# Kernel optimization log

Hardware: AMD Instinct MI355X
Metric: run time of the kernel (lower is better)

The kernel has to match this reference:

```python
import jax, jax.numpy as jnp
import numpy as np

B, D, H = 65536, 1024, 8
HD = D // H


def setup_inputs() -> dict:
    key = jax.random.key(0)
    ks = jax.random.split(key, 6)
    s = 0.02  # init scale for weights
    return {
        "feat_a": jax.random.normal(ks[0], (B, D), jnp.float32),
        "feat_b": jax.random.normal(ks[1], (B, D), jnp.float32),
        "w_in_ab": jax.random.normal(ks[2], (3 * D, D), jnp.float32) * s,
        "b_in_ab": jnp.zeros((3 * D,), jnp.float32),
        "w_out_ab": jax.random.normal(ks[3], (D, D), jnp.float32) * s,
        "b_out_ab": jnp.zeros((D,), jnp.float32),
        "w_in_ba": jax.random.normal(ks[4], (3 * D, D), jnp.float32) * s,
        "b_in_ba": jnp.zeros((3 * D,), jnp.float32),
        "w_out_ba": jax.random.normal(ks[5], (D, D), jnp.float32) * s,
        "b_out_ba": jnp.zeros((D,), jnp.float32),
    }


def _mha_len1(q_in, kv_in, w_in, b_in, w_out, b_out):
    """PyTorch nn.MultiheadAttention math specialized to seq_len == 1 (eval mode).
    q_in, kv_in: [B, D]. Returns [B, D]."""
    wq, wk, wv = w_in[:D], w_in[D:2 * D], w_in[2 * D:]
    bq, bk, bv = b_in[:D], b_in[D:2 * D], b_in[2 * D:]
    q = q_in @ wq.T + bq                      # [B, D]
    k = kv_in @ wk.T + bk                     # [B, D]
    v = kv_in @ wv.T + bv                     # [B, D]
    qh = q.reshape(-1, H, HD)
    kh = k.reshape(-1, H, HD)
    vh = v.reshape(-1, H, HD)
    scores = jnp.sum(qh * kh, axis=-1) / jnp.sqrt(jnp.float32(HD))  # [B, H]
    # softmax over key axis of length 1 -> all ones; kept explicit for fidelity
    attn = jax.nn.softmax(scores[:, :, None], axis=-1)              # [B, H, 1]
    ctx = (attn * vh).reshape(-1, D)                                # [B, D]
    return ctx @ w_out.T + b_out


def reference(feat_a, feat_b, w_in_ab, b_in_ab, w_out_ab, b_out_ab,
              w_in_ba, b_in_ba, w_out_ba, b_out_ba):
    attended_a = _mha_len1(feat_a, feat_b, w_in_ab, b_in_ab, w_out_ab, b_out_ab)
    attended_b = _mha_len1(feat_b, feat_a, w_in_ba, b_in_ba, w_out_ba, b_out_ba)
    return jnp.concatenate([attended_a, attended_b], axis=-1)  # [B, 2D]
```

## Files before the change

kernel.cpp:

```cpp
#include <hip/hip_runtime.h>
#include <hip/hip_bf16.h>
#include <stdint.h>

#define D_DIM 1024
#define B_ROWS 65536
#define BM 128
#define BN 128
#define BK 32

typedef __bf16 bf16x8 __attribute__((ext_vector_type(8)));
typedef float f32x4 __attribute__((ext_vector_type(4)));

__device__ inline uint32_t pack_bf16(float x, float y) {
  union { float f; uint32_t u; } ax, ay;
  ax.f = x; ay.f = y;
  uint32_t ux = ax.u + 0x7FFFu + ((ax.u >> 16) & 1u);
  uint32_t uy = ay.u + 0x7FFFu + ((ay.u >> 16) & 1u);
  return (ux >> 16) | (uy & 0xFFFF0000u);
}

__device__ inline uint16_t f32_to_bf16_rne(float x) {
  union { float f; uint32_t u; } v; v.f = x;
  uint32_t u = v.u + 0x7FFFu + ((v.u >> 16) & 1u);
  return (uint16_t)(u >> 16);
}

__global__ __launch_bounds__(256) void combine_w_kernel(
    const float* __restrict__ w_in_ab, const float* __restrict__ w_out_ab,
    const float* __restrict__ w_in_ba, const float* __restrict__ w_out_ba,
    uint16_t* __restrict__ M_ab, uint16_t* __restrict__ M_ba)
{
  const int z = blockIdx.z;
  const float* WO = z ? w_out_ba : w_out_ab;
  const float* WV = (z ? w_in_ba : w_in_ab) + 2 * D_DIM * D_DIM;
  uint16_t* M = z ? M_ba : M_ab;

  const int n0 = blockIdx.y * 64, k0 = blockIdx.x * 64;
  __shared__ float As[64][17];
  __shared__ float Bs[16][65];
  const int t = threadIdx.x;
  const int tx = t & 15, ty = t >> 4;

  float acc[4][4] = {};
  for (int j0 = 0; j0 < D_DIM; j0 += 16) {
    {
      int r = t >> 2, c = (t & 3) * 4;
      const float* src = WO + (uint64_t)(n0 + r) * D_DIM + j0 + c;
      As[r][c + 0] = src[0]; As[r][c + 1] = src[1];
      As[r][c + 2] = src[2]; As[r][c + 3] = src[3];
    }
    {
      int r = t >> 4, c = (t & 15) * 4;
      const float* src = WV + (uint64_t)(j0 + r) * D_DIM + k0 + c;
      Bs[r][c + 0] = src[0]; Bs[r][c + 1] = src[1];
      Bs[r][c + 2] = src[2]; Bs[r][c + 3] = src[3];
    }
    __syncthreads();
#pragma unroll
    for (int kk = 0; kk < 16; ++kk) {
      float a[4], b[4];
#pragma unroll
      for (int i = 0; i < 4; ++i) a[i] = As[ty * 4 + i][kk];
#pragma unroll
      for (int j = 0; j < 4; ++j) b[j] = Bs[kk][tx * 4 + j];
#pragma unroll
      for (int i = 0; i < 4; ++i)
#pragma unroll
        for (int j = 0; j < 4; ++j)
          acc[i][j] = fmaf(a[i], b[j], acc[i][j]);
    }
    __syncthreads();
  }
#pragma unroll
  for (int i = 0; i < 4; ++i)
#pragma unroll
    for (int j = 0; j < 4; ++j)
      M[(uint64_t)(n0 + ty * 4 + i) * D_DIM + k0 + tx * 4 + j] =
          f32_to_bf16_rne(acc[i][j]);
}

__global__ __launch_bounds__(256) void combine_bias_kernel(
    const float* __restrict__ w_out_ab, const float* __restrict__ b_in_ab,
    const float* __restrict__ b_out_ab,
    const float* __restrict__ w_out_ba, const float* __restrict__ b_in_ba,
    const float* __restrict__ b_out_ba,
    float* __restrict__ bias_ab, float* __restrict__ bias_ba)
{
  const int z = blockIdx.y;
  const float* WO  = z ? w_out_ba : w_out_ab;
  const float* bin = (z ? b_in_ba : b_in_ab) + 2 * D_DIM;
  const float* bo  = z ? b_out_ba : b_out_ab;
  float* bias = z ? bias_ba : bias_ab;

  const int n = blockIdx.x, t = threadIdx.x;
  float p = 0.f;
  for (int j = t; j < D_DIM; j += 256)
    p += WO[(uint64_t)n * D_DIM + j] * bin[j];
  for (int off = 32; off; off >>= 1) p += __shfl_down(p, off, 64);
  __shared__ float ws[4];
  if ((t & 63) == 0) ws[t >> 6] = p;
  __syncthreads();
  if (t == 0) bias[n] = ws[0] + ws[1] + ws[2] + ws[3] + bo[n];
}

__global__ __launch_bounds__(256, 2) void gemm_main(
    const float* __restrict__ feat_a, const float* __restrict__ feat_b,
    const uint16_t* __restrict__ M_ab, const uint16_t* __restrict__ M_ba,
    const float* __restrict__ bias_ab, const float* __restrict__ bias_ba,
    float* __restrict__ out)
{
  const int z = blockIdx.z;
  const float* A = z ? feat_a : feat_b;
  const uint16_t* W = z ? M_ba : M_ab;
  const float* bias = z ? bias_ba : bias_ab;
  const int m0 = blockIdx.y * BM;
  const int n0 = blockIdx.x * BN;
  const int col_off = z * D_DIM;

  __shared__ __align__(16) uint16_t As[BM * BK];
  __shared__ __align__(16) uint16_t Bs[BN * BK];

  const int t = threadIdx.x;
  const int lane = t & 63, wave = t >> 6;
  const int wm = wave >> 1, wn = wave & 1;
  const int lr = lane & 15, lq = lane >> 4;

  f32x4 acc[4][4] = {};

  const int ar = t >> 1, ac = (t & 1) * 16;
  const float* ag = A + (uint64_t)(m0 + ar) * D_DIM + ac;
  uint4* as_dst = (uint4*)As + t * 2;

  const int br = t >> 1, bc = (t & 1) * 16;
  const uint16_t* bg = W + (uint64_t)(n0 + br) * D_DIM + bc;
  uint4* bs_dst = (uint4*)Bs + t * 2;

  const uint4* asv = (const uint4*)As;
  const uint4* bsv = (const uint4*)Bs;

  for (int k0 = 0; k0 < D_DIM; k0 += BK) {
    __syncthreads();
    {
      const float4* src = (const float4*)(ag + k0);
      float4 f0 = src[0], f1 = src[1], f2 = src[2], f3 = src[3];
      uint4 w0; uint4 w1;
      w0.x = pack_bf16(f0.x, f0.y); w0.y = pack_bf16(f0.z, f0.w);
      w0.z = pack_bf16(f1.x, f1.y); w0.w = pack_bf16(f1.z, f1.w);
      w1.x = pack_bf16(f2.x, f2.y); w1.y = pack_bf16(f2.z, f2.w);
      w1.z = pack_bf16(f3.x, f3.y); w1.w = pack_bf16(f3.z, f3.w);
      as_dst[0] = w0; as_dst[1] = w1;
    }
    {
      const uint4* src = (const uint4*)(bg + k0);
      uint4 b0 = src[0], b1 = src[1];
      bs_dst[0] = b0; bs_dst[1] = b1;
    }
    __syncthreads();

    bf16x8 afrag[4], bfrag[4];
#pragma unroll
    for (int mt = 0; mt < 4; ++mt)
      afrag[mt] = __builtin_bit_cast(bf16x8, asv[(wm * 64 + mt * 16 + lr) * 4 + lq]);
#pragma unroll
    for (int nt = 0; nt < 4; ++nt)
      bfrag[nt] = __builtin_bit_cast(bf16x8, bsv[(wn * 64 + nt * 16 + lr) * 4 + lq]);
#pragma unroll
    for (int mt = 0; mt < 4; ++mt)
#pragma unroll
      for (int nt = 0; nt < 4; ++nt)
        acc[mt][nt] = __builtin_amdgcn_mfma_f32_16x16x32_bf16(
            afrag[mt], bfrag[nt], acc[mt][nt], 0, 0, 0);
  }

#pragma unroll
  for (int nt = 0; nt < 4; ++nt) {
    const int col = n0 + wn * 64 + nt * 16 + lr;
    const float bv = bias[col];
#pragma unroll
    for (int mt = 0; mt < 4; ++mt) {
      const int row = m0 + wm * 64 + mt * 16 + lq * 4;
      float* op = out + (uint64_t)row * (2 * D_DIM) + col_off + col;
#pragma unroll
      for (int r = 0; r < 4; ++r)
        op[(uint64_t)r * (2 * D_DIM)] = acc[mt][nt][r] + bv;
    }
  }
}

extern "C" void kernel_launch(void* const* d_in, const int* in_sizes, int n_in,
                              void* d_out, int out_size, void* d_ws, size_t ws_size,
                              hipStream_t stream) {
  const float* feat_a   = (const float*)d_in[0];
  const float* feat_b   = (const float*)d_in[1];
  const float* w_in_ab  = (const float*)d_in[2];
  const float* b_in_ab  = (const float*)d_in[3];
  const float* w_out_ab = (const float*)d_in[4];
  const float* b_out_ab = (const float*)d_in[5];
  const float* w_in_ba  = (const float*)d_in[6];
  const float* b_in_ba  = (const float*)d_in[7];
  const float* w_out_ba = (const float*)d_in[8];
  const float* b_out_ba = (const float*)d_in[9];
  float* out = (float*)d_out;

  uint8_t* ws = (uint8_t*)d_ws;
  uint16_t* M_ab  = (uint16_t*)(ws);
  uint16_t* M_ba  = (uint16_t*)(ws + (2u << 20));
  float*    bias_ab = (float*)(ws + (4u << 20));
  float*    bias_ba = (float*)(ws + (4u << 20) + 4096);

  combine_w_kernel<<<dim3(16, 16, 2), 256, 0, stream>>>(
      w_in_ab, w_out_ab, w_in_ba, w_out_ba, M_ab, M_ba);
  combine_bias_kernel<<<dim3(1024, 2), 256, 0, stream>>>(
      w_out_ab, b_in_ab, b_out_ab, w_out_ba, b_in_ba, b_out_ba,
      bias_ab, bias_ba);
  gemm_main<<<dim3(D_DIM / BN, B_ROWS / BM, 2), 256, 0, stream>>>(
      feat_a, feat_b, M_ab, M_ba, bias_ab, bias_ba, out);
}
```

Measured before the change: 1.405 ms.

## Pre-convert features to bf16, DMA tiles to LDS, XCD-aware 256x128 GEMM tiling

When the workspace is large enough, a separate pass converts both fp32 feature matrices to bf16. The main GEMM then loads A and W tiles straight into LDS with global_load_lds, which drops the per-iteration fp32 loads and in-loop packing. The GEMM tile grows to 256x128, and blocks are remapped so all eight N-tiles of one M-tile land on the same XCD, to improve L2 reuse of A. The weight fold becomes an MFMA GEMM using a hi/lo bf16 split for accuracy. The conversion pass adds extra full-size memory traffic, and the fast path depends on ws_size, with a fallback path kept.

```diff
diff --git a/kernel.cpp b/kernel.cpp
--- a/kernel.cpp
+++ b/kernel.cpp
@@ -1,31 +1,56 @@
 #include <hip/hip_runtime.h>
-#include <hip/hip_bf16.h>
 #include <stdint.h>
 
 #define D_DIM 1024
 #define B_ROWS 65536
-#define BM 128
-#define BN 128
-#define BK 32
 
 typedef __bf16 bf16x8 __attribute__((ext_vector_type(8)));
 typedef float f32x4 __attribute__((ext_vector_type(4)));
 
-__device__ inline uint32_t pack_bf16(float x, float y) {
-  union { float f; uint32_t u; } ax, ay;
-  ax.f = x; ay.f = y;
-  uint32_t ux = ax.u + 0x7FFFu + ((ax.u >> 16) & 1u);
-  uint32_t uy = ay.u + 0x7FFFu + ((ay.u >> 16) & 1u);
-  return (ux >> 16) | (uy & 0xFFFF0000u);
-}
-
-__device__ inline uint16_t f32_to_bf16_rne(float x) {
+typedef __attribute__((address_space(1))) uint8_t ga_u8;
+typedef __attribute__((address_space(3))) uint8_t lds_u8;
+
+__device__ __forceinline__ void dma16(const void* g, void* l) {
+  __builtin_amdgcn_global_load_lds((ga_u8*)(uintptr_t)g,
+                                   (lds_u8*)(uint32_t)(uintptr_t)l, 16, 0, 0);
+}
+
+__device__ __forceinline__ uint16_t bf16_rne(float x) {
   union { float f; uint32_t u; } v; v.f = x;
   uint32_t u = v.u + 0x7FFFu + ((v.u >> 16) & 1u);
   return (uint16_t)(u >> 16);
 }
-
-__global__ __launch_bounds__(256) void combine_w_kernel(
+__device__ __forceinline__ float bf16_f32(uint16_t h) {
+  union { uint32_t u; float f; } v; v.u = (uint32_t)h << 16;
+  return v.f;
+}
+__device__ __forceinline__ uint32_t pk2(float x, float y) {
+  return (uint32_t)bf16_rne(x) | ((uint32_t)bf16_rne(y) << 16);
+}
+__device__ __forceinline__ void split2(float x, uint16_t& h, uint16_t& l) {
+  h = bf16_rne(x);
+  l = bf16_rne(x - bf16_f32(h));
+}
+
+__global__ __launch_bounds__(256) void conv_kernel(
+    const float* __restrict__ fa, const float* __restrict__ fb,
+    uint16_t* __restrict__ o0, uint16_t* __restrict__ o1)
+{
+  const uint32_t HALFT = 8388608u;
+  uint32_t i = blockIdx.x * 256 + threadIdx.x;
+  const float* s; uint16_t* d; uint32_t t;
+  if (i < HALFT) { s = fb; d = o0; t = i; }
+  else           { s = fa; d = o1; t = i - HALFT; }
+  uint64_t e = (uint64_t)t * 8;
+  const float4* sp = (const float4*)(s + e);
+  float4 f0 = sp[0], f1 = sp[1];
+  uint4 w;
+  w.x = pk2(f0.x, f0.y); w.y = pk2(f0.z, f0.w);
+  w.z = pk2(f1.x, f1.y); w.w = pk2(f1.z, f1.w);
+  *(uint4*)(d + e) = w;
+}
+
+__global__ __launch_bounds__(256) void fold_w(
     const float* __restrict__ w_in_ab, const float* __restrict__ w_out_ab,
     const float* __restrict__ w_in_ba, const float* __restrict__ w_out_ba,
     uint16_t* __restrict__ M_ab, uint16_t* __restrict__ M_ba)
@@ -34,52 +59,102 @@
   const float* WO = z ? w_out_ba : w_out_ab;
   const float* WV = (z ? w_in_ba : w_in_ab) + 2 * D_DIM * D_DIM;
   uint16_t* M = z ? M_ba : M_ab;
-
-  const int n0 = blockIdx.y * 64, k0 = blockIdx.x * 64;
-  __shared__ float As[64][17];
-  __shared__ float Bs[16][65];
-  const int t = threadIdx.x;
-  const int tx = t & 15, ty = t >> 4;
-
-  float acc[4][4] = {};
-  for (int j0 = 0; j0 < D_DIM; j0 += 16) {
+  const int n0 = blockIdx.y * 128, k0 = blockIdx.x * 128;
+
+  __shared__ __align__(16) uint16_t Ah[128 * 32], Al[128 * 32];
+  __shared__ __align__(16) uint16_t Bh[128 * 32], Bl[128 * 32];
+
+  const int t = threadIdx.x, lane = t & 63, w = t >> 6;
+  const int wm = w >> 1, wn = w & 1;
+  const int lr = lane & 15, lq = lane >> 4;
+
+  f32x4 acc[4][4] = {};
+
+  const int ar = t >> 1, ac = (t & 1) * 16;
+  const float* ag = WO + (uint64_t)(n0 + ar) * D_DIM + ac;
+  const int bj = t >> 3, bc = (t & 7) * 16;
+  const float* bgp = WV + (uint64_t)bj * D_DIM + k0 + bc;
+
+  for (int j0 = 0; j0 < D_DIM; j0 += 32) {
+    __syncthreads();
     {
-      int r = t >> 2, c = (t & 3) * 4;
-      const float* src = WO + (uint64_t)(n0 + r) * D_DIM + j0 + c;
-      As[r][c + 0] = src[0]; As[r][c + 1] = src[1];
-      As[r][c + 2] = src[2]; As[r][c + 3] = src[3];
+      float av[16];
+      const float4* s = (const float4*)(ag + j0);
+#pragma unroll
+      for (int q = 0; q < 4; ++q) {
+        float4 f = s[q];
+        av[4*q] = f.x; av[4*q+1] = f.y; av[4*q+2] = f.z; av[4*q+3] = f.w;
+      }
+      uint16_t hh[16], ll[16];
+#pragma unroll
+      for (int i = 0; i < 16; ++i) split2(av[i], hh[i], ll[i]);
+      uint4* dh = (uint4*)(Ah + t * 16);
+      uint4* dl = (uint4*)(Al + t * 16);
+#pragma unroll
+      for (int q = 0; q < 2; ++q) {
+        uint4 vh, vl;
+        vh.x = (uint32_t)hh[8*q+0] | ((uint32_t)hh[8*q+1] << 16);
+        vh.y = (uint32_t)hh[8*q+2] | ((uint32_t)hh[8*q+3] << 16);
+        vh.z = (uint32_t)hh[8*q+4] | ((uint32_t)hh[8*q+5] << 16);
+        vh.w = (uint32_t)hh[8*q+6] | ((uint32_t)hh[8*q+7] << 16);
+        vl.x = (uint32_t)ll[8*q+0] | ((uint32_t)ll[8*q+1] << 16);
+        vl.y = (uint32_t)ll[8*q+2] | ((uint32_t)ll[8*q+3] << 16);
+        vl.z = (uint32_t)ll[8*q+4] | ((uint32_t)ll[8*q+5] << 16);
+        vl.w = (uint32_t)ll[8*q+6] | ((uint32_t)ll[8*q+7] << 16);
+        dh[q] = vh; dl[q] = vl;
+      }
     }
     {
-      int r = t >> 4, c = (t & 15) * 4;
-      const float* src = WV + (uint64_t)(j0 + r) * D_DIM + k0 + c;
-      Bs[r][c + 0] = src[0]; Bs[r][c + 1] = src[1];
-      Bs[r][c + 2] = src[2]; Bs[r][c + 3] = src[3];
+      const float* s = bgp + (uint64_t)j0 * D_DIM;
+#pragma unroll
+      for (int i = 0; i < 16; ++i) {
+        float x = s[i];
+        uint16_t h, l; split2(x, h, l);
+        Bh[(bc + i) * 32 + bj] = h;
+        Bl[(bc + i) * 32 + bj] = l;
+      }
     }
     __syncthreads();
-#pragma unroll
-    for (int kk = 0; kk < 16; ++kk) {
-      float a[4], b[4];
-#pragma unroll
-      for (int i = 0; i < 4; ++i) a[i] = As[ty * 4 + i][kk];
-#pragma unroll
-      for (int j = 0; j < 4; ++j) b[j] = Bs[kk][tx * 4 + j];
-#pragma unroll
-      for (int i = 0; i < 4; ++i)
-#pragma unroll
-        for (int j = 0; j < 4; ++j)
-          acc[i][j] = fmaf(a[i], b[j], acc[i][j]);
-    }
-    __syncthreads();
-  }
-#pragma unroll
-  for (int i = 0; i < 4; ++i)
-#pragma unroll
-    for (int j = 0; j < 4; ++j)
-      M[(uint64_t)(n0 + ty * 4 + i) * D_DIM + k0 + tx * 4 + j] =
-          f32_to_bf16_rne(acc[i][j]);
-}
-
-__global__ __launch_bounds__(256) void combine_bias_kernel(
+
+    bf16x8 ah[4], al[4], bh[4], bl[4];
+    const uint4* avh = (const uint4*)Ah; const uint4* avl = (const uint4*)Al;
+    const uint4* bvh = (const uint4*)Bh; const uint4* bvl = (const uint4*)Bl;
+#pragma unroll
+    for (int mt = 0; mt < 4; ++mt) {
+      int r = (wm * 64 + mt * 16 + lr) * 4 + lq;
+      ah[mt] = __builtin_bit_cast(bf16x8, avh[r]);
+      al[mt] = __builtin_bit_cast(bf16x8, avl[r]);
+    }
+#pragma unroll
+    for (int nt = 0; nt < 4; ++nt) {
+      int r = (wn * 64 + nt * 16 + lr) * 4 + lq;
+      bh[nt] = __builtin_bit_cast(bf16x8, bvh[r]);
+      bl[nt] = __builtin_bit_cast(bf16x8, bvl[r]);
+    }
+#pragma unroll
+    for (int mt = 0; mt < 4; ++mt)
+#pragma unroll
+      for (int nt = 0; nt < 4; ++nt) {
+        acc[mt][nt] = __builtin_amdgcn_mfma_f32_16x16x32_bf16(ah[mt], bh[nt], acc[mt][nt], 0, 0, 0);
+        acc[mt][nt] = __builtin_amdgcn_mfma_f32_16x16x32_bf16(ah[mt], bl[nt], acc[mt][nt], 0, 0, 0);
+        acc[mt][nt] = __builtin_amdgcn_mfma_f32_16x16x32_bf16(al[mt], bh[nt], acc[mt][nt], 0, 0, 0);
+      }
+  }
+
+#pragma unroll
+  for (int nt = 0; nt < 4; ++nt) {
+    const int col = k0 + wn * 64 + nt * 16 + lr;
+#pragma unroll
+    for (int mt = 0; mt < 4; ++mt) {
+      const int rowb = n0 + wm * 64 + mt * 16 + lq * 4;
+#pragma unroll
+      for (int r = 0; r < 4; ++r)
+        M[(uint64_t)(rowb + r) * D_DIM + col] = bf16_rne(acc[mt][nt][r]);
+    }
+  }
+}
+
+__global__ __launch_bounds__(256) void fold_bias(
     const float* __restrict__ w_out_ab, const float* __restrict__ b_in_ab,
     const float* __restrict__ b_out_ab,
     const float* __restrict__ w_out_ba, const float* __restrict__ b_in_ba,
@@ -103,82 +178,92 @@
   if (t == 0) bias[n] = ws[0] + ws[1] + ws[2] + ws[3] + bo[n];
 }
 
+template <bool PRECONV>
 __global__ __launch_bounds__(256, 2) void gemm_main(
-    const float* __restrict__ feat_a, const float* __restrict__ feat_b,
+    const void* __restrict__ A0, const void* __restrict__ A1,
     const uint16_t* __restrict__ M_ab, const uint16_t* __restrict__ M_ba,
     const float* __restrict__ bias_ab, const float* __restrict__ bias_ba,
     float* __restrict__ out)
 {
-  const int z = blockIdx.z;
-  const float* A = z ? feat_a : feat_b;
+  const uint32_t lin = blockIdx.x;
+  const uint32_t xcd = lin & 7, j = (lin >> 3) & 7, g = lin >> 6;
+  const uint32_t mp = g * 8 + xcd;
+  const uint32_t z  = mp >> 8;
+  const uint32_t m0 = (mp & 255) * 256;
+  const uint32_t n0 = j * 128;
+
+  const void* Aany = z ? A1 : A0;
   const uint16_t* W = z ? M_ba : M_ab;
   const float* bias = z ? bias_ba : bias_ab;
-  const int m0 = blockIdx.y * BM;
-  const int n0 = blockIdx.x * BN;
-  const int col_off = z * D_DIM;
-
-  __shared__ __align__(16) uint16_t As[BM * BK];
-  __shared__ __align__(16) uint16_t Bs[BN * BK];
-
-  const int t = threadIdx.x;
-  const int lane = t & 63, wave = t >> 6;
-  const int wm = wave >> 1, wn = wave & 1;
+
+  __shared__ __align__(16) uint16_t As[256 * 32];
+  __shared__ __align__(16) uint16_t Bs[128 * 32];
+
+  const int t = threadIdx.x, lane = t & 63, w = t >> 6;
+  const int wm = w >> 1, wn = w & 1;
   const int lr = lane & 15, lq = lane >> 4;
 
-  f32x4 acc[4][4] = {};
-
-  const int ar = t >> 1, ac = (t & 1) * 16;
-  const float* ag = A + (uint64_t)(m0 + ar) * D_DIM + ac;
-  uint4* as_dst = (uint4*)As + t * 2;
-
-  const int br = t >> 1, bc = (t & 1) * 16;
-  const uint16_t* bg = W + (uint64_t)(n0 + br) * D_DIM + bc;
-  uint4* bs_dst = (uint4*)Bs + t * 2;
-
-  const uint4* asv = (const uint4*)As;
-  const uint4* bsv = (const uint4*)Bs;
-
-  for (int k0 = 0; k0 < D_DIM; k0 += BK) {
+  f32x4 acc[8][4] = {};
+
+  const int qrow = lane >> 2;
+  const int qcol = (lane & 3) * 8;
+  const uint16_t* abf = (const uint16_t*)Aany;
+  const uint16_t* ag  = abf + (uint64_t)(m0 + w * 64 + qrow) * D_DIM + qcol;
+  uint16_t* al0 = As + w * 2048 + lane * 8;
+  const uint16_t* bg = W + (uint64_t)(n0 + w * 32 + qrow) * D_DIM + qcol;
+  uint16_t* bl0 = Bs + w * 1024 + lane * 8;
+
+  const float* afp = (const float*)Aany + (uint64_t)(m0 + t) * D_DIM;
+
+  for (int k0 = 0; k0 < D_DIM; k0 += 32) {
     __syncthreads();
-    {
-      const float4* src = (const float4*)(ag + k0);
-      float4 f0 = src[0], f1 = src[1], f2 = src[2], f3 = src[3];
-      uint4 w0; uint4 w1;
-      w0.x = pack_bf16(f0.x, f0.y); w0.y = pack_bf16(f0.z, f0.w);
-      w0.z = pack_bf16(f1.x, f1.y); w0.w = pack_bf16(f1.z, f1.w);
-      w1.x = pack_bf16(f2.x, f2.y); w1.y = pack_bf16(f2.z, f2.w);
-      w1.z = pack_bf16(f3.x, f3.y); w1.w = pack_bf16(f3.z, f3.w);
-      as_dst[0] = w0; as_dst[1] = w1;
-    }
-    {
-      const uint4* src = (const uint4*)(bg + k0);
-      uint4 b0 = src[0], b1 = src[1];
-      bs_dst[0] = b0; bs_dst[1] = b1;
-    }
+    if constexpr (PRECONV) {
+#pragma unroll
+      for (int q = 0; q < 4; ++q)
+        dma16(ag + k0 + q * 16 * D_DIM, al0 + q * 512);
+    } else {
+      const float4* src = (const float4*)(afp + k0);
+      float4 f[8];
+#pragma unroll
+      for (int q = 0; q < 8; ++q) f[q] = src[q];
+      uint4* dst = (uint4*)(As + t * 32);
+#pragma unroll
+      for (int q = 0; q < 4; ++q) {
+        uint4 wv;
+        wv.x = pk2(f[2*q].x,   f[2*q].y);   wv.y = pk2(f[2*q].z,   f[2*q].w);
+        wv.z = pk2(f[2*q+1].x, f[2*q+1].y); wv.w = pk2(f[2*q+1].z, f[2*q+1].w);
+        dst[q] = wv;
+      }
+    }
+#pragma unroll
+    for (int q = 0; q < 2; ++q)
+      dma16(bg + k0 + q * 16 * D_DIM, bl0 + q * 512);
     __syncthreads();
 
-    bf16x8 afrag[4], bfrag[4];
-#pragma unroll
-    for (int mt = 0; mt < 4; ++mt)
-      afrag[mt] = __builtin_bit_cast(bf16x8, asv[(wm * 64 + mt * 16 + lr) * 4 + lq]);
+    bf16x8 a[8], b[4];
+    const uint4* asv = (const uint4*)As;
+    const uint4* bsv = (const uint4*)Bs;
+#pragma unroll
+    for (int mt = 0; mt < 8; ++mt)
+      a[mt] = __builtin_bit_cast(bf16x8, asv[(wm * 128 + mt * 16 + lr) * 4 + lq]);
 #pragma unroll
     for (int nt = 0; nt < 4; ++nt)
-      bfrag[nt] = __builtin_bit_cast(bf16x8, bsv[(wn * 64 + nt * 16 + lr) * 4 + lq]);
-#pragma unroll
-    for (int mt = 0; mt < 4; ++mt)
+      b[nt] = __builtin_bit_cast(bf16x8, bsv[(wn * 64 + nt * 16 + lr) * 4 + lq]);
+#pragma unroll
+    for (int mt = 0; mt < 8; ++mt)
 #pragma unroll
       for (int nt = 0; nt < 4; ++nt)
-        acc[mt][nt] = __builtin_amdgcn_mfma_f32_16x16x32_bf16(
-            afrag[mt], bfrag[nt], acc[mt][nt], 0, 0, 0);
-  }
-
+        acc[mt][nt] = __builtin_amdgcn_mfma_f32_16x16x32_bf16(a[mt], b[nt], acc[mt][nt], 0, 0, 0);
+  }
+
+  const uint32_t col_off = z * D_DIM;
 #pragma unroll
   for (int nt = 0; nt < 4; ++nt) {
     const int col = n0 + wn * 64 + nt * 16 + lr;
     const float bv = bias[col];
 #pragma unroll
-    for (int mt = 0; mt < 4; ++mt) {
-      const int row = m0 + wm * 64 + mt * 16 + lq * 4;
+    for (int mt = 0; mt < 8; ++mt) {
+      const int row = m0 + wm * 128 + mt * 16 + lq * 4;
       float* op = out + (uint64_t)row * (2 * D_DIM) + col_off + col;
 #pragma unroll
       for (int r = 0; r < 4; ++r)
@@ -203,16 +288,38 @@
   float* out = (float*)d_out;
 
   uint8_t* ws = (uint8_t*)d_ws;
-  uint16_t* M_ab  = (uint16_t*)(ws);
-  uint16_t* M_ba  = (uint16_t*)(ws + (2u << 20));
-  float*    bias_ab = (float*)(ws + (4u << 20));
-  float*    bias_ba = (float*)(ws + (4u << 20) + 4096);
-
-  combine_w_kernel<<<dim3(16, 16, 2), 256, 0, stream>>>(
+  const size_t FEAT_B2 = (size_t)B_ROWS * D_DIM * 2;
+  const size_t need = 2 * FEAT_B2 + (4u << 20) + 8192;
+  const bool big = ws_size >= need;
+
+  uint16_t *A0 = nullptr, *A1 = nullptr, *M_ab, *M_ba;
+  float *bias_ab, *bias_ba;
+  if (big) {
+    A0 = (uint16_t*)ws;
+    A1 = (uint16_t*)(ws + FEAT_B2);
+    M_ab = (uint16_t*)(ws + 2 * FEAT_B2);
+    M_ba = (uint16_t*)(ws + 2 * FEAT_B2 + (2u << 20));
+    bias_ab = (float*)(ws + 2 * FEAT_B2 + (4u << 20));
+    bias_ba = (float*)(ws + 2 * FEAT_B2 + (4u << 20) + 4096);
+  } else {
+    M_ab = (uint16_t*)ws;
+    M_ba = (uint16_t*)(ws + (2u << 20));
+    bias_ab = (float*)(ws + (4u << 20));
+    bias_ba = (float*)(ws + (4u << 20) + 4096);
+  }
+
+  fold_w<<<dim3(8, 8, 2), 256, 0, stream>>>(
       w_in_ab, w_out_ab, w_in_ba, w_out_ba, M_ab, M_ba);
-  combine_bias_kernel<<<dim3(1024, 2), 256, 0, stream>>>(
+  fold_bias<<<dim3(1024, 2), 256, 0, stream>>>(
       w_out_ab, b_in_ab, b_out_ab, w_out_ba, b_in_ba, b_out_ba,
       bias_ab, bias_ba);
-  gemm_main<<<dim3(D_DIM / BN, B_ROWS / BM, 2), 256, 0, stream>>>(
-      feat_a, feat_b, M_ab, M_ba, bias_ab, bias_ba, out);
-}
+
+  if (big) {
+    conv_kernel<<<65536, 256, 0, stream>>>(feat_a, feat_b, A0, A1);
+    gemm_main<true><<<4096, 256, 0, stream>>>(
+        A0, A1, M_ab, M_ba, bias_ab, bias_ba, out);
+  } else {
+    gemm_main<false><<<4096, 256, 0, stream>>>(
+        feat_b, feat_a, M_ab, M_ba, bias_ab, bias_ba, out);
+  }
+}
```

Result: faster. 1.317 ms (-6.3%).
